# Kernel tuning notes

Hardware: AMD Instinct MI355X
Metric: run time of the kernel (lower is better)

Reference implementation:

```python
import jax, jax.numpy as jnp
import numpy as np

WINDOW = 11
PAD = WINDOW // 2
C1 = 0.01 ** 2
C2 = 0.03 ** 2


def _avg_pool(x):
    # Matches torch F.avg_pool2d(x, k, stride=1, padding=k//2) with
    # count_include_pad=True (default): sum over zero-padded window / k^2.
    # Separable box filter: sum over H then W.
    s = jax.lax.reduce_window(
        x, 0.0, jax.lax.add,
        window_dimensions=(1, 1, WINDOW, 1), window_strides=(1, 1, 1, 1),
        padding=((0, 0), (0, 0), (PAD, PAD), (0, 0)))
    s = jax.lax.reduce_window(
        s, 0.0, jax.lax.add,
        window_dimensions=(1, 1, 1, WINDOW), window_strides=(1, 1, 1, 1),
        padding=((0, 0), (0, 0), (0, 0), (PAD, PAD)))
    return s * (1.0 / (WINDOW * WINDOW))


def setup_inputs() -> dict:
    key = jax.random.key(0)
    k1, k2 = jax.random.split(key)
    shape = (16, 3, 512, 512)
    pred = jax.random.uniform(k1, shape, dtype=jnp.float32)
    target = jax.random.uniform(k2, shape, dtype=jnp.float32)
    return {"pred": pred, "target": target}


def reference(pred, target):
    mu_x = _avg_pool(pred)
    mu_y = _avg_pool(target)
    mu_x_sq = mu_x * mu_x
    mu_y_sq = mu_y * mu_y
    mu_xy = mu_x * mu_y
    sigma_x = _avg_pool(pred * pred) - mu_x_sq
    sigma_y = _avg_pool(target * target) - mu_y_sq
    sigma_xy = _avg_pool(pred * target) - mu_xy
    ssim_map = ((2.0 * mu_xy + C1) * (2.0 * sigma_xy + C2)
                / ((mu_x_sq + mu_y_sq + C1) * (sigma_x + sigma_y + C2)))
    ssim_map = jnp.clip(ssim_map, 0.0, 1.0)
    # per-sample loss: 1 - mean over C,H,W
    return 1.0 - jnp.mean(ssim_map.reshape(ssim_map.shape[0], -1), axis=1)
```

## Files before the change

### kernel.cpp

```cpp
#include <hip/hip_runtime.h>

#define HH 512
#define WW 512
#define NCH 3
#define NBATCH 16
#define NIMG (NBATCH*NCH)
#define CHUNK 64
#define NCHUNK (HH/CHUNK)
#define NSTRIP 4
#define SW 128
#define SLOTS 140
#define NT 64

static __device__ __forceinline__ float2 f2add(float2 a, float2 b){ return make_float2(a.x+b.x, a.y+b.y); }

struct RowData { float4 m; float2 h; };

__global__ __launch_bounds__(NT) void ssim_main(
    const float* __restrict__ pred, const float* __restrict__ targ,
    float* __restrict__ ws)
{
  __shared__ __align__(16) float2 rowb[SLOTS];
  __shared__ __align__(16) float4 ring0[11][NT];
  __shared__ __align__(16) float4 ring1[11][NT];

  const int l = threadIdx.x;
  const int blk = blockIdx.x;
  const int img = blk >> 5;
  const int rem = blk & 31;
  const int chunk = rem >> 2;
  const int strip = rem & 3;
  const int b = img / NCH;

  const int r0 = chunk*CHUNK - 5;
  const int c0 = strip*SW;

  if (l < 10) rowb[(l < 5) ? l : (128 + l)] = make_float2(0.f, 0.f);
  asm volatile("" ::: "memory");

  const size_t ib = (size_t)img * (size_t)(HH*WW);
  const float* pp = pred + ib;
  const float* tp = targ + ib;

  const int cm = c0 + 2*l;
  const int h  = l - 54;
  const int ch = (h < 5) ? (c0 - 5 + h) : (c0 + 123 + h);
  const bool hval = (l >= 54) && ((unsigned)ch < (unsigned)WW);
  const int hs = (h < 5) ? h : (128 + h);

  auto loadrow = [&](int it) -> RowData {
    RowData d;
    const int r = r0 + it;
    if ((unsigned)r < (unsigned)HH) {
      const size_t ro = (size_t)r * WW;
      const float2 x = *(const float2*)(pp + ro + cm);
      const float2 y = *(const float2*)(tp + ro + cm);
      d.m = make_float4(x.x, x.y, y.x, y.y);
      if (hval) d.h = make_float2(pp[ro + ch], tp[ro + ch]);
      else      d.h = make_float2(0.f, 0.f);
    } else {
      d.m = make_float4(0.f, 0.f, 0.f, 0.f);
      d.h = make_float2(0.f, 0.f);
    }
    return d;
  };

  float2 vx = make_float2(0.f,0.f), vy = vx, vxy = vx, vss = vx;
  float acc = 0.f;

  RowData cur = loadrow(0);
  RowData nxt = loadrow(1);
  RowData nx2 = loadrow(2);

  constexpr float c1 = 0.0001f, c2 = 0.0009f, inv121 = 1.0f/121.0f;

  auto ssim1 = [&](float Sx, float Sy, float Sxy, float Sss) -> float {
    const float mux = Sx*inv121, muy = Sy*inv121;
    const float muxy = mux*muy;
    const float m2   = fmaf(mux, mux, muy*muy);
    const float sgxy = fmaf(Sxy, inv121, -muxy);
    const float sgss = fmaf(Sss, inv121, -m2);
    const float num = fmaf(2.f, muxy, c1) * fmaf(2.f, sgxy, c2);
    const float den = (m2 + c1) * (sgss + c2);
    const float s = num * __builtin_amdgcn_rcpf(den);
    return fminf(fmaxf(s, 0.f), 1.f);
  };

  auto body = [&](int it, int slot, bool dosub, bool doemit) {
    rowb[5 + 2*l] = make_float2(cur.m.x, cur.m.z);
    rowb[6 + 2*l] = make_float2(cur.m.y, cur.m.w);
    if (hval) rowb[hs] = cur.h;
    cur = nxt; nxt = nx2;
    nx2 = loadrow(it + 3);
    asm volatile("" ::: "memory");

    const float4* tb = (const float4*)(rowb + 2*l);
    float sx=0.f, sy=0.f, sxy=0.f, sss=0.f;
    float x0=0.f, y0=0.f, x11=0.f, y11=0.f;
    #pragma unroll
    for (int j = 0; j < 6; ++j) {
      const float4 v = tb[j];
      if (j == 0) { x0 = v.x; y0 = v.y; }
      sx += v.x; sy += v.y;
      sxy = fmaf(v.x, v.y, sxy);
      sss = fmaf(v.x, v.x, sss);
      sss = fmaf(v.y, v.y, sss);
      if (j < 5) {
        sx += v.z; sy += v.w;
        sxy = fmaf(v.z, v.w, sxy);
        sss = fmaf(v.z, v.z, sss);
        sss = fmaf(v.w, v.w, sss);
      } else { x11 = v.z; y11 = v.w; }
    }

    const float2 hx  = make_float2(sx,  sx - x0 + x11);
    const float2 hy  = make_float2(sy,  sy - y0 + y11);
    const float2 hxy = make_float2(sxy, fmaf(x11, y11, fmaf(-x0, y0, sxy)));
    const float2 hss = make_float2(sss,
        fmaf(x11, x11, fmaf(y11, y11, fmaf(-x0, x0, fmaf(-y0, y0, sss)))));

    if (dosub) {
      const float4 o0 = ring0[slot][l];
      const float4 o1 = ring1[slot][l];
      vx.x  -= o0.x; vx.y  -= o1.x;
      vy.x  -= o0.y; vy.y  -= o1.y;
      vxy.x -= o0.z; vxy.y -= o1.z;
      vss.x -= o0.w; vss.y -= o1.w;
    }
    ring0[slot][l] = make_float4(hx.x, hy.x, hxy.x, hss.x);
    ring1[slot][l] = make_float4(hx.y, hy.y, hxy.y, hss.y);
    asm volatile("" ::: "memory");

    vx  = f2add(vx,  hx);  vy  = f2add(vy,  hy);
    vxy = f2add(vxy, hxy); vss = f2add(vss, hss);

    if (doemit) {
      acc += ssim1(vx.x, vy.x, vxy.x, vss.x);
      acc += ssim1(vx.y, vy.y, vxy.y, vss.y);
    }
  };

  #pragma unroll
  for (int u = 0; u < 11; ++u) body(u, u, false, u == 10);
  for (int g = 0; g < 5; ++g) {
    #pragma unroll
    for (int u = 0; u < 11; ++u) body(11 + 11*g + u, u, true, true);
  }
  #pragma unroll
  for (int u = 0; u < 8; ++u) body(66 + u, u, true, true);

  #pragma unroll
  for (int off = 32; off > 0; off >>= 1) acc += __shfl_down(acc, off, 64);
  if (l == 0) atomicAdd(&ws[b], acc);
}

__global__ void ssim_final(const float* __restrict__ ws, float* __restrict__ out) {
  const int i = threadIdx.x;
  if (i < NBATCH) out[i] = 1.0f - ws[i] * (1.0f / (float)(NCH*HH*WW));
}

extern "C" void kernel_launch(void* const* d_in, const int* in_sizes, int n_in,
                              void* d_out, int out_size, void* d_ws, size_t ws_size,
                              hipStream_t stream) {
  const float* pred = (const float*)d_in[0];
  const float* targ = (const float*)d_in[1];
  float* out = (float*)d_out;
  float* ws  = (float*)d_ws;
  hipMemsetAsync(ws, 0, NBATCH * sizeof(float), stream);
  ssim_main<<<dim3(NIMG*NCHUNK*NSTRIP), dim3(NT), 0, stream>>>(pred, targ, ws);
  ssim_final<<<dim3(1), dim3(64), 0, stream>>>(ws, out);
}
```

Before: 173.7 us.

## Software-pipeline LDS tap and ring reads one row ahead of compute

The per-row body is split into a stage that stores the current row to LDS and reads the next row's six taps and ring entries, and a compute stage that consumes taps already held in registers. The row loop is fully unrolled over all 74 rows, and the compiler memory fences are removed so LDS latency can overlap with arithmetic. A waves-per-EU hint of 1 is added so the compiler may use more registers for the extra live values. The risk is higher register pressure and lower occupancy, which would hide global-load latency less well.

```diff
diff --git a/kernel.cpp b/kernel.cpp
--- a/kernel.cpp
+++ b/kernel.cpp
@@ -11,12 +11,13 @@
 #define SW 128
 #define SLOTS 140
 #define NT 64
-
-static __device__ __forceinline__ float2 f2add(float2 a, float2 b){ return make_float2(a.x+b.x, a.y+b.y); }
+#define NROWS (CHUNK+10)
 
 struct RowData { float4 m; float2 h; };
+struct Taps { float4 v[6]; };
 
-__global__ __launch_bounds__(NT) void ssim_main(
+__global__ __launch_bounds__(NT) __attribute__((amdgpu_waves_per_eu(1)))
+void ssim_main(
     const float* __restrict__ pred, const float* __restrict__ targ,
     float* __restrict__ ws)
 {
@@ -36,7 +37,6 @@
   const int c0 = strip*SW;
 
   if (l < 10) rowb[(l < 5) ? l : (128 + l)] = make_float2(0.f, 0.f);
-  asm volatile("" ::: "memory");
 
   const size_t ib = (size_t)img * (size_t)(HH*WW);
   const float* pp = pred + ib;
@@ -86,20 +86,26 @@
     return fminf(fmaxf(s, 0.f), 1.f);
   };
 
-  auto body = [&](int it, int slot, bool dosub, bool doemit) {
+  auto stage_issue = [&](int it) -> Taps {
     rowb[5 + 2*l] = make_float2(cur.m.x, cur.m.z);
     rowb[6 + 2*l] = make_float2(cur.m.y, cur.m.w);
     if (hval) rowb[hs] = cur.h;
     cur = nxt; nxt = nx2;
     nx2 = loadrow(it + 3);
-    asm volatile("" ::: "memory");
+    Taps t;
+    const float4* tb = (const float4*)(rowb + 2*l);
+    #pragma unroll
+    for (int j = 0; j < 6; ++j) t.v[j] = tb[j];
+    return t;
+  };
 
-    const float4* tb = (const float4*)(rowb + 2*l);
+  auto compute = [&](const Taps& t, const float4& o0, const float4& o1,
+                     int slot, bool dosub, bool doemit) {
     float sx=0.f, sy=0.f, sxy=0.f, sss=0.f;
     float x0=0.f, y0=0.f, x11=0.f, y11=0.f;
     #pragma unroll
     for (int j = 0; j < 6; ++j) {
-      const float4 v = tb[j];
+      const float4 v = t.v[j];
       if (j == 0) { x0 = v.x; y0 = v.y; }
       sx += v.x; sy += v.y;
       sxy = fmaf(v.x, v.y, sxy);
@@ -112,7 +118,6 @@
         sss = fmaf(v.w, v.w, sss);
       } else { x11 = v.z; y11 = v.w; }
     }
-
     const float2 hx  = make_float2(sx,  sx - x0 + x11);
     const float2 hy  = make_float2(sy,  sy - y0 + y11);
     const float2 hxy = make_float2(sxy, fmaf(x11, y11, fmaf(-x0, y0, sxy)));
@@ -120,8 +125,6 @@
         fmaf(x11, x11, fmaf(y11, y11, fmaf(-x0, x0, fmaf(-y0, y0, sss)))));
 
     if (dosub) {
-      const float4 o0 = ring0[slot][l];
-      const float4 o1 = ring1[slot][l];
       vx.x  -= o0.x; vx.y  -= o1.x;
       vy.x  -= o0.y; vy.y  -= o1.y;
       vxy.x -= o0.z; vxy.y -= o1.z;
@@ -129,10 +132,9 @@
     }
     ring0[slot][l] = make_float4(hx.x, hy.x, hxy.x, hss.x);
     ring1[slot][l] = make_float4(hx.y, hy.y, hxy.y, hss.y);
-    asm volatile("" ::: "memory");
 
-    vx  = f2add(vx,  hx);  vy  = f2add(vy,  hy);
-    vxy = f2add(vxy, hxy); vss = f2add(vss, hss);
+    vx.x += hx.x; vx.y += hx.y;  vy.x += hy.x; vy.y += hy.y;
+    vxy.x += hxy.x; vxy.y += hxy.y;  vss.x += hss.x; vss.y += hss.y;
 
     if (doemit) {
       acc += ssim1(vx.x, vy.x, vxy.x, vss.x);
@@ -140,14 +142,25 @@
     }
   };
 
+  Taps tc = stage_issue(0);
+  float4 oc0 = make_float4(0.f,0.f,0.f,0.f), oc1 = oc0;
   #pragma unroll
-  for (int u = 0; u < 11; ++u) body(u, u, false, u == 10);
-  for (int g = 0; g < 5; ++g) {
-    #pragma unroll
-    for (int u = 0; u < 11; ++u) body(11 + 11*g + u, u, true, true);
+  for (int it = 0; it < NROWS; ++it) {
+    const int slot   = (it < 11) ? it : (it - 11) % 11;
+    const bool dosub = (it >= 11);
+    const bool doemit= (it >= 10);
+    Taps tn;
+    float4 no0 = make_float4(0.f,0.f,0.f,0.f), no1 = no0;
+    if (it + 1 < NROWS) {
+      tn = stage_issue(it + 1);
+      if (it + 1 >= 11) {
+        const int ns = (it + 1 - 11) % 11;
+        no0 = ring0[ns][l]; no1 = ring1[ns][l];
+      }
+    }
+    compute(tc, oc0, oc1, slot, dosub, doemit);
+    tc = tn; oc0 = no0; oc1 = no1;
   }
-  #pragma unroll
-  for (int u = 0; u < 8; ++u) body(66 + u, u, true, true);
 
   #pragma unroll
   for (int off = 32; off > 0; off >>= 1) acc += __shfl_down(acc, off, 64);
```

Result: slower. 385.6 us (+122.0%).
